# Kernel optimization log

Measured on AMD Instinct MI355X. Metric: run time of the kernel, lower is better.

The kernel has to match this reference:

```python
import jax, jax.numpy as jnp
import numpy as np
import math

HIDDEN = 1024
N_HEADS = 16
N_KV = 4
HEAD_DIM = HIDDEN // N_HEADS  # 64
B, S = 2, 2048
THETA = 100000.0


def _freqs_cos_sin(dim, end, theta):
    # yarn params: original_max_position_embeddings=2048 >= end, so no ramp scaling,
    # attention_factor=1.0 -> plain RoPE frequencies.
    inv = 1.0 / theta ** (np.arange(0, dim, 2)[: dim // 2] / dim)
    t = np.arange(end)
    f = np.outer(t, inv).astype(np.float32)  # (end, dim/2)
    cos = np.concatenate([np.cos(f), np.cos(f)], axis=-1)  # (end, dim)
    sin = np.concatenate([np.sin(f), np.sin(f)], axis=-1)
    return jnp.asarray(cos), jnp.asarray(sin)


def _rotate(x):
    # stack([-x[...,1::2], x[...,::2]], -1).reshape_as(x)
    return jnp.stack([-x[..., 1::2], x[..., ::2]], axis=-1).reshape(x.shape)


def setup_inputs() -> dict:
    key = jax.random.key(0)
    ks = jax.random.split(key, 9)
    s = 0.02
    return {
        "hidden_states": jax.random.normal(ks[0], (B, S, HIDDEN), jnp.float32),
        "attention_mask": jnp.ones((B, S), jnp.int32),
        "Wq": jax.random.normal(ks[1], (HIDDEN, HIDDEN), jnp.float32) * s,
        "bq": jnp.zeros((HIDDEN,), jnp.float32),
        "Wk": jax.random.normal(ks[2], (HIDDEN, N_KV * HEAD_DIM), jnp.float32) * s,
        "bk": jnp.zeros((N_KV * HEAD_DIM,), jnp.float32),
        "Wv": jax.random.normal(ks[3], (HIDDEN, N_KV * HEAD_DIM), jnp.float32) * s,
        "bv": jnp.zeros((N_KV * HEAD_DIM,), jnp.float32),
        "Wo": jax.random.normal(ks[4], (HIDDEN, HIDDEN), jnp.float32) * s,
        "bo": jnp.zeros((HIDDEN,), jnp.float32),
    }


def reference(hidden_states, attention_mask, Wq, bq, Wk, bk, Wv, bv, Wo, bo):
    b, s, _ = hidden_states.shape
    q = (hidden_states @ Wq + bq).reshape(b, s, N_HEADS, HEAD_DIM)
    k = (hidden_states @ Wk + bk).reshape(b, s, N_KV, HEAD_DIM)
    v = (hidden_states @ Wv + bv).reshape(b, s, N_KV, HEAD_DIM)

    cos, sin = _freqs_cos_sin(HEAD_DIM, s, THETA)
    cos = cos[:, None, :]  # (s,1,d) broadcasts over (b,s,h,d)
    sin = sin[:, None, :]
    q = q * cos + _rotate(q) * sin
    k = k * cos + _rotate(k) * sin

    # GQA: repeat_interleave kv heads -> jnp.repeat along head axis
    rep = N_HEADS // N_KV
    k = jnp.repeat(k, rep, axis=2)
    v = jnp.repeat(v, rep, axis=2)

    scores = jnp.einsum("bqhd,bkhd->bhqk", q, k) / math.sqrt(HEAD_DIM)
    neg = jnp.finfo(scores.dtype).min
    causal = jnp.triu(jnp.ones((s, s), bool), k=1)  # (q,kv)
    bias = jnp.where(causal, neg, 0.0).astype(scores.dtype)[None, None]
    key_mask = attention_mask.astype(bool)[:, None, None, :]  # (b,1,1,kv)
    bias = jnp.where(key_mask, bias, neg)
    probs = jax.nn.softmax(scores + bias, axis=-1)
    attn = jnp.einsum("bhqk,bkhd->bqhd", probs, v).reshape(b, s, HIDDEN)
    return attn @ Wo + bo
```

## Files before the change

kernel.cpp:

```cpp
#include <hip/hip_runtime.h>
#include <cstddef>
#include <cstdint>

#define B_   2
#define S_   2048
#define HID  1024
#define NH_  16
#define NKV_ 4
#define DH_  64
#define ROWS (B_ * S_)
#define NQKV 1536
#define QSCALE 0.18033688011112042f

typedef __bf16 bf16_t;
typedef _Float16 f16_t;
typedef bf16_t bf16x8 __attribute__((ext_vector_type(8)));
typedef bf16_t bf16x4 __attribute__((ext_vector_type(4)));
typedef f16_t  f16x8  __attribute__((ext_vector_type(8)));
typedef f16_t  f16x4  __attribute__((ext_vector_type(4)));
typedef float  f32x4  __attribute__((ext_vector_type(4)));

typedef __attribute__((address_space(1))) const uint32_t gu32_t;
typedef __attribute__((address_space(3))) uint32_t lu32_t;

__device__ __forceinline__ void gl_lds16(const void* g, void* l) {
  __builtin_amdgcn_global_load_lds((gu32_t*)g, (lu32_t*)l, 16, 0, 0);
}

__global__ void prep_all(const float* __restrict__ hs,
                         const float* __restrict__ Wq, const float* __restrict__ Wk,
                         const float* __restrict__ Wv, const float* __restrict__ Wo,
                         const float* __restrict__ bq, const float* __restrict__ bk,
                         const float* __restrict__ bv,
                         bf16_t* __restrict__ hsb,
                         bf16_t* __restrict__ Wt, bf16_t* __restrict__ Wot,
                         float* __restrict__ ball, float2* __restrict__ lut)
{
  const int bid = blockIdx.x;
  if (bid < 2048) {
    const int i = (bid * 256 + threadIdx.x) * 8;
    float4 a = *(const float4*)(hs + i);
    float4 b = *(const float4*)(hs + i + 4);
    bf16x8 o;
    o[0]=(bf16_t)a.x; o[1]=(bf16_t)a.y; o[2]=(bf16_t)a.z; o[3]=(bf16_t)a.w;
    o[4]=(bf16_t)b.x; o[5]=(bf16_t)b.y; o[6]=(bf16_t)b.z; o[7]=(bf16_t)b.w;
    *(bf16x8*)(hsb + i) = o;
    return;
  }
  if (bid >= 4614) {
    const int idx = (bid - 4614) * 256 + threadIdx.x;
    const int s = idx >> 5, j = idx & 31;
    const float L = 0.51905126482615037f;
    const float ang = (float)s * exp2f(-L * (float)j);
    lut[idx] = make_float2(cosf(ang), sinf(ang));
    return;
  }
  if (bid >= 4608) {
    int i = (bid - 4608) * 256 + threadIdx.x;
    if (i < NQKV) ball[i] = (i < 1024) ? bq[i] : ((i < 1280) ? bk[i-1024] : bv[i-1280]);
    return;
  }
  const int wb = bid - 2048;
  const float* src; bf16_t* dst; int N, n0, k0;
  if (wb < 1024)      { src = Wq; dst = Wt;            N = 1024; int t = wb;      n0=(t&31)*32; k0=(t>>5)*32; }
  else if (wb < 1280) { src = Wk; dst = Wt + 1024*HID; N = 256;  int t = wb-1024; n0=(t&7)*32;  k0=(t>>3)*32; }
  else if (wb < 1536) { src = Wv; dst = Wt + 1280*HID; N = 256;  int t = wb-1280; n0=(t&7)*32;  k0=(t>>3)*32; }
  else                { src = Wo; dst = Wot;           N = 1024; int t = wb-1536; n0=(t&31)*32; k0=(t>>5)*32; }
  __shared__ bf16_t T[32][33];
  const int tx = threadIdx.x & 31, ty = threadIdx.x >> 5;
#pragma unroll
  for (int i = 0; i < 4; ++i)
    T[ty + i*8][tx] = (bf16_t)src[(size_t)(k0 + ty + i*8) * N + n0 + tx];
  __syncthreads();
#pragma unroll
  for (int i = 0; i < 4; ++i)
    dst[(size_t)(n0 + ty + i*8) * HID + k0 + tx] = T[tx][ty + i*8];
}

__global__ __launch_bounds__(256, 3) void gemm64_b16o(
    const bf16_t* __restrict__ A, const bf16_t* __restrict__ Bt,
    const float* __restrict__ bias, bf16_t* __restrict__ C, int N)
{
  __shared__ bf16_t As[2][128 * 64];
  __shared__ bf16_t Bs[2][64 * 64];
  const int tid  = threadIdx.x;
  const int w    = tid >> 6;
  const int lane = tid & 63;
  const int m    = lane & 15;
  const int quad = lane >> 4;
  const int wm   = w >> 1, wn = w & 1;
  const size_t bm = (size_t)blockIdx.y * 128;
  const size_t bn = (size_t)blockIdx.x * 64;

  const int srow = w * 8 + (lane >> 3);
  const int scol = (lane & 7) * 8;
  const bf16_t* Ag = A  + (bm + srow) * HID + scol;
  const bf16_t* Bg = Bt + (bn + srow) * HID + scol;

  f32x4 acc[4][2];
#pragma unroll
  for (int i = 0; i < 4; ++i)
#pragma unroll
    for (int j = 0; j < 2; ++j) acc[i][j] = (f32x4){0.f, 0.f, 0.f, 0.f};

#pragma unroll
  for (int i = 0; i < 4; ++i)
    gl_lds16(Ag + (size_t)(i * 32) * HID, &As[0][(w * 8 + i * 32) * 64]);
#pragma unroll
  for (int i = 0; i < 2; ++i)
    gl_lds16(Bg + (size_t)(i * 32) * HID, &Bs[0][(w * 8 + i * 32) * 64]);

  int p = 0;
  for (int k0 = 0; k0 < HID; k0 += 64) {
    __syncthreads();
    if (k0 + 64 < HID) {
#pragma unroll
      for (int i = 0; i < 4; ++i)
        gl_lds16(Ag + (size_t)(i * 32) * HID + k0 + 64, &As[p^1][(w * 8 + i * 32) * 64]);
#pragma unroll
      for (int i = 0; i < 2; ++i)
        gl_lds16(Bg + (size_t)(i * 32) * HID + k0 + 64, &Bs[p^1][(w * 8 + i * 32) * 64]);
    }
#pragma unroll
    for (int ks = 0; ks < 2; ++ks) {
      bf16x8 af[4], bfr[2];
#pragma unroll
      for (int mt = 0; mt < 4; ++mt)
        af[mt] = *(const bf16x8*)&As[p][(wm * 64 + mt * 16 + m) * 64 + ks * 32 + quad * 8];
#pragma unroll
      for (int nt = 0; nt < 2; ++nt)
        bfr[nt] = *(const bf16x8*)&Bs[p][(wn * 32 + nt * 16 + m) * 64 + ks * 32 + quad * 8];
#pragma unroll
      for (int mt = 0; mt < 4; ++mt)
#pragma unroll
        for (int nt = 0; nt < 2; ++nt)
          acc[mt][nt] = __builtin_amdgcn_mfma_f32_16x16x32_bf16(bfr[nt], af[mt], acc[mt][nt], 0, 0, 0);
    }
    p ^= 1;
  }
#pragma unroll
  for (int mt = 0; mt < 4; ++mt) {
    const size_t row = bm + wm * 64 + mt * 16 + m;
#pragma unroll
    for (int nt = 0; nt < 2; ++nt) {
      const size_t col = bn + wn * 32 + nt * 16 + quad * 4;
      float4 bb = *(const float4*)&bias[col];
      bf16x4 o;
      o[0] = (bf16_t)(acc[mt][nt][0] + bb.x);
      o[1] = (bf16_t)(acc[mt][nt][1] + bb.y);
      o[2] = (bf16_t)(acc[mt][nt][2] + bb.z);
      o[3] = (bf16_t)(acc[mt][nt][3] + bb.w);
      *(bf16x4*)&C[row * N + col] = o;
    }
  }
}

__global__ __launch_bounds__(256, 3) void gemm64_f32o(
    const bf16_t* __restrict__ A, const bf16_t* __restrict__ Bt,
    const float* __restrict__ bias, float* __restrict__ C, int N)
{
  __shared__ bf16_t As[2][128 * 64];
  __shared__ bf16_t Bs[2][64 * 64];
  const int tid  = threadIdx.x;
  const int w    = tid >> 6;
  const int lane = tid & 63;
  const int m    = lane & 15;
  const int quad = lane >> 4;
  const int wm   = w >> 1, wn = w & 1;
  const size_t bm = (size_t)blockIdx.y * 128;
  const size_t bn = (size_t)blockIdx.x * 64;

  const int srow = w * 8 + (lane >> 3);
  const int scol = (lane & 7) * 8;
  const bf16_t* Ag = A  + (bm + srow) * HID + scol;
  const bf16_t* Bg = Bt + (bn + srow) * HID + scol;

  f32x4 acc[4][2];
#pragma unroll
  for (int i = 0; i < 4; ++i)
#pragma unroll
    for (int j = 0; j < 2; ++j) acc[i][j] = (f32x4){0.f, 0.f, 0.f, 0.f};

#pragma unroll
  for (int i = 0; i < 4; ++i)
    gl_lds16(Ag + (size_t)(i * 32) * HID, &As[0][(w * 8 + i * 32) * 64]);
#pragma unroll
  for (int i = 0; i < 2; ++i)
    gl_lds16(Bg + (size_t)(i * 32) * HID, &Bs[0][(w * 8 + i * 32) * 64]);

  int p = 0;
  for (int k0 = 0; k0 < HID; k0 += 64) {
    __syncthreads();
    if (k0 + 64 < HID) {
#pragma unroll
      for (int i = 0; i < 4; ++i)
        gl_lds16(Ag + (size_t)(i * 32) * HID + k0 + 64, &As[p^1][(w * 8 + i * 32) * 64]);
#pragma unroll
      for (int i = 0; i < 2; ++i)
        gl_lds16(Bg + (size_t)(i * 32) * HID + k0 + 64, &Bs[p^1][(w * 8 + i * 32) * 64]);
    }
#pragma unroll
    for (int ks = 0; ks < 2; ++ks) {
      bf16x8 af[4], bfr[2];
#pragma unroll
      for (int mt = 0; mt < 4; ++mt)
        af[mt] = *(const bf16x8*)&As[p][(wm * 64 + mt * 16 + m) * 64 + ks * 32 + quad * 8];
#pragma unroll
      for (int nt = 0; nt < 2; ++nt)
        bfr[nt] = *(const bf16x8*)&Bs[p][(wn * 32 + nt * 16 + m) * 64 + ks * 32 + quad * 8];
#pragma unroll
      for (int mt = 0; mt < 4; ++mt)
#pragma unroll
        for (int nt = 0; nt < 2; ++nt)
          acc[mt][nt] = __builtin_amdgcn_mfma_f32_16x16x32_bf16(bfr[nt], af[mt], acc[mt][nt], 0, 0, 0);
    }
    p ^= 1;
  }
#pragma unroll
  for (int mt = 0; mt < 4; ++mt) {
    const size_t row = bm + wm * 64 + mt * 16 + m;
#pragma unroll
    for (int nt = 0; nt < 2; ++nt) {
      const size_t col = bn + wn * 32 + nt * 16 + quad * 4;
      float4 bb = *(const float4*)&bias[col];
      float4 o;
      o.x = acc[mt][nt][0] + bb.x; o.y = acc[mt][nt][1] + bb.y;
      o.z = acc[mt][nt][2] + bb.z; o.w = acc[mt][nt][3] + bb.w;
      *(float4*)&C[row * N + col] = o;
    }
  }
}

__global__ void prep_kv(const bf16_t* __restrict__ QKVb, const float2* __restrict__ lut,
                        bf16_t* __restrict__ Kimg, f16_t* __restrict__ Vimg)
{
  __shared__ bf16_t Lk[64][72];
  __shared__ bf16_t Lv[64][72];
  const int bid = blockIdx.x, t = threadIdx.x;
  const int kt = bid & 31, kvh = (bid >> 5) & 3, b = bid >> 7;
  const size_t img = ((size_t)(b * NKV_ + kvh) * 32 + kt) * 4096;

  {
    const int r0 = t >> 3, c8 = (t & 7) * 8;
#pragma unroll
    for (int i = 0; i < 2; ++i) {
      const int r = r0 + i * 32;
      const bf16_t* src = QKVb + (size_t)(b * S_ + kt * 64 + r) * NQKV + 1024 + kvh * DH_ + c8;
      *(bf16x8*)&Lk[r][c8] = *(const bf16x8*)src;
      *(bf16x8*)&Lv[r][c8] = *(const bf16x8*)(src + 256);
    }
  }
  __syncthreads();
  {
    const int key = t & 63, cg = t >> 6;
    const int srow = kt * 64 + key;
    bf16x8 a = *(const bf16x8*)&Lk[key][cg * 16];
    bf16x8 c = *(const bf16x8*)&Lk[key][cg * 16 + 8];
    const float2* lp = lut + srow * 32 + ((cg & 1) * 16);
    float v[16];
#pragma unroll
    for (int i = 0; i < 8; ++i) { v[i] = (float)a[i]; v[i + 8] = (float)c[i]; }
    bf16x8 o0, o1;
#pragma unroll
    for (int j = 0; j < 8; ++j) {
      const float2 ce = lp[2 * j], co = lp[2 * j + 1];
      const float y0 = v[2*j] * ce.x - v[2*j+1] * ce.y;
      const float y1 = v[2*j+1] * co.x + v[2*j] * co.y;
      if (j < 4) { o0[2*j] = (bf16_t)y0; o0[2*j+1] = (bf16_t)y1; }
      else       { o1[2*(j-4)] = (bf16_t)y0; o1[2*(j-4)+1] = (bf16_t)y1; }
    }
    const int s0 = (2 * cg) ^ (key & 7);
    *(bf16x8*)&Kimg[img + key * 64 + s0 * 8]       = o0;
    *(bf16x8*)&Kimg[img + key * 64 + (s0 ^ 1) * 8] = o1;
  }
  {
    const int d = t & 63, cg = t >> 6;
#pragma unroll
    for (int g4 = 0; g4 < 4; ++g4) {
      const int g = cg * 4 + g4;
      f16x4 o;
#pragma unroll
      for (int j = 0; j < 4; ++j)
        o[j] = (f16_t)(float)Lv[g * 4 + j][d];
      const int slot = g ^ (d & 15);
      *(f16x4*)&Vimg[img + d * 64 + slot * 4] = o;
    }
  }
}

__global__ __launch_bounds__(256, 4) void attn_v7(
    const bf16_t* __restrict__ QKVb, const float2* __restrict__ lut,
    const bf16_t* __restrict__ Kt2, const f16_t* __restrict__ Vt2,
    const int* __restrict__ amask, bf16_t* __restrict__ Ab)
{
  __shared__ __align__(16) bf16_t Ks[2][64 * 64];
  __shared__ __align__(16) f16_t  Vs[2][64 * 64];

  const int tid  = threadIdx.x;
  const int w    = tid >> 6;
  const int lane = tid & 63;
  const int m    = lane & 15;
  const int quad = lane >> 4;
  const int kvh  = blockIdx.y;
  const int b    = blockIdx.z;
  const int h    = kvh * 4 + w;
  const int qt   = 127 - blockIdx.x;
  const int q0w  = qt * 16;
  const int nkt  = (q0w >> 6) + 1;

  bf16x8 aq[2];
  {
    const int spos = q0w + m;
    const bf16_t* qsrc = QKVb + (size_t)(b * S_ + spos) * NQKV + h * DH_;
    float2 l8[8];
#pragma unroll
    for (int j = 0; j < 8; ++j) l8[j] = lut[spos * 32 + quad * 8 + j];
#pragma unroll
    for (int kc = 0; kc < 2; ++kc) {
      bf16x8 x = *(const bf16x8*)(qsrc + kc * 32 + quad * 8);
      bf16x8 y;
#pragma unroll
      for (int i = 0; i < 4; ++i) {
        const float x0 = (float)x[2*i], x1 = (float)x[2*i+1];
        y[2*i]   = (bf16_t)((x0 * l8[2*i].x   - x1 * l8[2*i].y)   * QSCALE);
        y[2*i+1] = (bf16_t)((x1 * l8[2*i+1].x + x0 * l8[2*i+1].y) * QSCALE);
      }
      aq[kc] = y;
    }
  }

  f32x4 oacc[4];
#pragma unroll
  for (int d = 0; d < 4; ++d) oacc[d] = (f32x4){0.f,0.f,0.f,0.f};
  float lpart = 0.f;

  const size_t imgbase = ((size_t)(b * NKV_ + kvh) * 32) * 4096;
  const bf16_t* Kg = Kt2 + imgbase;
  const f16_t*  Vg = Vt2 + imgbase;
  const int x0s = quad ^ (m & 7);
  const int x1s = (4 + quad) ^ (m & 7);
  const int* amp = amask + b * S_;

  gl_lds16(Kg + (2*w)   * 512 + lane * 8, &Ks[0][(2*w)   * 512]);
  gl_lds16(Kg + (2*w+1) * 512 + lane * 8, &Ks[0][(2*w+1) * 512]);
  gl_lds16(Vg + (2*w)   * 512 + lane * 8, &Vs[0][(2*w)   * 512]);
  gl_lds16(Vg + (2*w+1) * 512 + lane * 8, &Vs[0][(2*w+1) * 512]);
  int mcur = amp[lane];

  int p = 0;
  for (int kt = 0; kt < nkt; ++kt) {
    const int kbase = kt * 64;
    __syncthreads();
    const bool more = (kt + 1 < nkt);
    if (more) {
      const size_t off = (size_t)(kt + 1) * 4096;
      gl_lds16(Kg + off + (2*w)   * 512 + lane * 8, &Ks[p^1][(2*w)   * 512]);
      gl_lds16(Kg + off + (2*w+1) * 512 + lane * 8, &Ks[p^1][(2*w+1) * 512]);
      gl_lds16(Vg + off + (2*w)   * 512 + lane * 8, &Vs[p^1][(2*w)   * 512]);
      gl_lds16(Vg + off + (2*w+1) * 512 + lane * 8, &Vs[p^1][(2*w+1) * 512]);
    }
    int mnext = more ? amp[(kt + 1) * 64 + lane] : 0;
    const uint64_t mb = __ballot(mcur != 0);

    f32x4 sc[4];
#pragma unroll
    for (int cb = 0; cb < 4; ++cb) sc[cb] = (f32x4){0.f,0.f,0.f,0.f};
#pragma unroll
    for (int cb = 0; cb < 4; ++cb) {
      const bf16x8 bk0 = *(const bf16x8*)&Ks[p][(cb*16 + m) * 64 + x0s * 8];
      const bf16x8 bk1 = *(const bf16x8*)&Ks[p][(cb*16 + m) * 64 + x1s * 8];
      sc[cb] = __builtin_amdgcn_mfma_f32_16x16x32_bf16(bk0, aq[0], sc[cb], 0, 0, 0);
      sc[cb] = __builtin_amdgcn_mfma_f32_16x16x32_bf16(bk1, aq[1], sc[cb], 0, 0, 0);
    }

    f16x4 bp[4];
    {
      const bool needm = (kbase + 63 > q0w) || (mb != ~0ull);
      if (needm) {
        const int qv = q0w + m;
#pragma unroll
        for (int cb = 0; cb < 4; ++cb)
#pragma unroll
          for (int r = 0; r < 4; ++r) {
            const int idx = cb*16 + quad*4 + r;
            const bool ok = (kbase + idx <= qv) && ((mb >> idx) & 1);
            sc[cb][r] = ok ? sc[cb][r] : -1e38f;
          }
      }
      float sum = 0.f;
#pragma unroll
      for (int cb = 0; cb < 4; ++cb) {
        f16x4 pp;
#pragma unroll
        for (int r = 0; r < 4; ++r) {
          const float pv = exp2f(sc[cb][r]);
          sum += pv;
          pp[r] = (f16_t)pv;
        }
        bp[cb] = pp;
      }
      lpart += sum;
    }

#pragma unroll
    for (int cb = 0; cb < 4; ++cb) {
      f16x4 av[4];
#pragma unroll
      for (int dblk = 0; dblk < 4; ++dblk) {
        const int slot = (cb * 4 + quad) ^ m;
        av[dblk] = *(const f16x4*)&Vs[p][(dblk*16 + m) * 64 + slot * 4];
      }
#pragma unroll
      for (int dblk = 0; dblk < 4; ++dblk)
        oacc[dblk] = __builtin_amdgcn_mfma_f32_16x16x16f16(av[dblk], bp[cb], oacc[dblk], 0, 0, 0);
    }
    mcur = mnext;
    p ^= 1;
  }

  {
    float l = lpart;
    l += __shfl_xor(l, 16);
    l += __shfl_xor(l, 32);
    const float inv = 1.0f / l;
    const size_t row = (size_t)(b * S_ + q0w + m);
#pragma unroll
    for (int dblk = 0; dblk < 4; ++dblk) {
      bf16x4 o;
      o[0] = (bf16_t)(oacc[dblk][0] * inv);
      o[1] = (bf16_t)(oacc[dblk][1] * inv);
      o[2] = (bf16_t)(oacc[dblk][2] * inv);
      o[3] = (bf16_t)(oacc[dblk][3] * inv);
      *(bf16x4*)&Ab[row * HID + h * DH_ + dblk * 16 + quad * 4] = o;
    }
  }
}

extern "C" void kernel_launch(void* const* d_in, const int* in_sizes, int n_in,
                              void* d_out, int out_size, void* d_ws, size_t ws_size,
                              hipStream_t stream)
{
  const float* hs    = (const float*)d_in[0];
  const int*   amask = (const int*)  d_in[1];
  const float* Wq    = (const float*)d_in[2];
  const float* bq    = (const float*)d_in[3];
  const float* Wk    = (const float*)d_in[4];
  const float* bk    = (const float*)d_in[5];
  const float* Wv    = (const float*)d_in[6];
  const float* bv    = (const float*)d_in[7];
  const float* Wo    = (const float*)d_in[8];
  const float* bo    = (const float*)d_in[9];
  float* out = (float*)d_out;

  bf16_t* QKVb = (bf16_t*)d_ws;
  bf16_t* hsb  = QKVb + (size_t)ROWS * NQKV;
  bf16_t* Wt   = hsb + (size_t)ROWS * HID;
  bf16_t* Wot  = Wt + (size_t)NQKV * HID;
  float*  ball = (float*)(Wot + (size_t)HID * HID);
  bf16_t* Kimg = (bf16_t*)(ball + NQKV);
  f16_t*  Vimg = (f16_t*)(Kimg + (size_t)B_*NKV_*32*4096);
  float2* lut  = (float2*)(Vimg + (size_t)B_*NKV_*32*4096);
  bf16_t* Ab   = hsb;

  prep_all<<<4870, 256, 0, stream>>>(hs, Wq, Wk, Wv, Wo, bq, bk, bv,
                                     hsb, Wt, Wot, ball, lut);

  gemm64_b16o<<<dim3(NQKV/64, ROWS/128), 256, 0, stream>>>(hsb, Wt, ball, QKVb, NQKV);

  prep_kv<<<256, 256, 0, stream>>>(QKVb, lut, Kimg, Vimg);

  attn_v7<<<dim3(128, NKV_, B_), 256, 0, stream>>>(QKVb, lut, Kimg, Vimg, amask, Ab);

  gemm64_f32o<<<dim3(HID/64, ROWS/128), 256, 0, stream>>>(Ab, Wot, bo, out, HID);
}
```

Baseline: 198.7 us.

## Pair complementary causal query tiles per block and split KV across wave groups

The attention kernel now gives each block two query tiles, one short causal row x and its complement 127-x. This balances the number of KV tiles per block and halves the grid to 64x4x2 with 512 threads. The combined KV tile sequence of both query tiles is interleaved across two 4-wave groups, each with its own double-buffered LDS K/V staging. Both groups keep partial accumulators for both tiles, so the partial outputs and row sums are exchanged through LDS and merged before normalization and the final store. This is meant to remove the causal load imbalance and long tail, at the cost of doubled LDS use, more registers for two accumulator sets, and an extra reduction step through LDS.

New measurement: 187.9 us. -5.4%, faster.

```diff
diff --git a/kernel.cpp b/kernel.cpp
--- a/kernel.cpp
+++ b/kernel.cpp
@@ -288,51 +288,107 @@
   }
 }
 
-__global__ __launch_bounds__(256, 4) void attn_v7(
+#define PROC_TILE(AQ, OACC, LP, Q0W)                                          \
+  do {                                                                        \
+    f32x4 sc[4];                                                              \
+    _Pragma("unroll") for (int cb = 0; cb < 4; ++cb)                          \
+      sc[cb] = (f32x4){0.f, 0.f, 0.f, 0.f};                                   \
+    _Pragma("unroll") for (int cb = 0; cb < 4; ++cb) {                        \
+      const bf16x8 bk0 = *(const bf16x8*)&Ks[g][p][(cb*16 + m) * 64 + x0s * 8]; \
+      const bf16x8 bk1 = *(const bf16x8*)&Ks[g][p][(cb*16 + m) * 64 + x1s * 8]; \
+      sc[cb] = __builtin_amdgcn_mfma_f32_16x16x32_bf16(bk0, AQ[0], sc[cb], 0, 0, 0); \
+      sc[cb] = __builtin_amdgcn_mfma_f32_16x16x32_bf16(bk1, AQ[1], sc[cb], 0, 0, 0); \
+    }                                                                         \
+    f16x4 bp[4];                                                              \
+    {                                                                         \
+      const bool needm = (kbase + 63 > (Q0W)) || (mb != ~0ull);               \
+      if (needm) {                                                            \
+        const int qv = (Q0W) + m;                                             \
+        _Pragma("unroll") for (int cb = 0; cb < 4; ++cb)                      \
+          _Pragma("unroll") for (int r = 0; r < 4; ++r) {                     \
+            const int idx = cb*16 + quad*4 + r;                               \
+            const bool ok = (kbase + idx <= qv) && ((mb >> idx) & 1);         \
+            sc[cb][r] = ok ? sc[cb][r] : -1e38f;                              \
+          }                                                                   \
+      }                                                                       \
+      float sum = 0.f;                                                        \
+      _Pragma("unroll") for (int cb = 0; cb < 4; ++cb) {                      \
+        f16x4 pp;                                                             \
+        _Pragma("unroll") for (int r = 0; r < 4; ++r) {                       \
+          const float pv = exp2f(sc[cb][r]);                                  \
+          sum += pv;                                                          \
+          pp[r] = (f16_t)pv;                                                  \
+        }                                                                     \
+        bp[cb] = pp;                                                          \
+      }                                                                       \
+      LP += sum;                                                              \
+    }                                                                         \
+    _Pragma("unroll") for (int cb = 0; cb < 4; ++cb) {                        \
+      f16x4 av[4];                                                            \
+      _Pragma("unroll") for (int dblk = 0; dblk < 4; ++dblk) {                \
+        const int slot = (cb * 4 + quad) ^ m;                                 \
+        av[dblk] = *(const f16x4*)&Vs[g][p][(dblk*16 + m) * 64 + slot * 4];   \
+      }                                                                       \
+      _Pragma("unroll") for (int dblk = 0; dblk < 4; ++dblk)                  \
+        OACC[dblk] = __builtin_amdgcn_mfma_f32_16x16x16f16(av[dblk], bp[cb], OACC[dblk], 0, 0, 0); \
+    }                                                                         \
+  } while (0)
+
+__global__ __launch_bounds__(512, 4) void attn_v8(
     const bf16_t* __restrict__ QKVb, const float2* __restrict__ lut,
     const bf16_t* __restrict__ Kt2, const f16_t* __restrict__ Vt2,
     const int* __restrict__ amask, bf16_t* __restrict__ Ab)
 {
-  __shared__ __align__(16) bf16_t Ks[2][64 * 64];
-  __shared__ __align__(16) f16_t  Vs[2][64 * 64];
+  __shared__ __align__(16) bf16_t Ks[2][2][64 * 64];
+  __shared__ __align__(16) f16_t  Vs[2][2][64 * 64];
 
   const int tid  = threadIdx.x;
   const int w    = tid >> 6;
+  const int g    = w >> 2;
+  const int wl   = w & 3;
   const int lane = tid & 63;
   const int m    = lane & 15;
   const int quad = lane >> 4;
   const int kvh  = blockIdx.y;
   const int b    = blockIdx.z;
-  const int h    = kvh * 4 + w;
-  const int qt   = 127 - blockIdx.x;
-  const int q0w  = qt * 16;
-  const int nkt  = (q0w >> 6) + 1;
-
-  bf16x8 aq[2];
-  {
-    const int spos = q0w + m;
+  const int h    = kvh * 4 + wl;
+  const int x    = blockIdx.x;
+  const int q0wA = x * 16;
+  const int q0wB = (127 - x) * 16;
+  const int nA   = (x >> 2) + 1;
+  const int nB   = ((127 - x) >> 2) + 1;
+  const int T    = nA + nB;
+
+  bf16x8 aqA[2], aqB[2];
+#pragma unroll
+  for (int tt = 0; tt < 2; ++tt) {
+    const int q0w_t = tt ? q0wB : q0wA;
+    const int spos = q0w_t + m;
     const bf16_t* qsrc = QKVb + (size_t)(b * S_ + spos) * NQKV + h * DH_;
     float2 l8[8];
 #pragma unroll
     for (int j = 0; j < 8; ++j) l8[j] = lut[spos * 32 + quad * 8 + j];
 #pragma unroll
     for (int kc = 0; kc < 2; ++kc) {
-      bf16x8 x = *(const bf16x8*)(qsrc + kc * 32 + quad * 8);
+      bf16x8 xv = *(const bf16x8*)(qsrc + kc * 32 + quad * 8);
       bf16x8 y;
 #pragma unroll
       for (int i = 0; i < 4; ++i) {
-        const float x0 = (float)x[2*i], x1 = (float)x[2*i+1];
+        const float x0 = (float)xv[2*i], x1 = (float)xv[2*i+1];
         y[2*i]   = (bf16_t)((x0 * l8[2*i].x   - x1 * l8[2*i].y)   * QSCALE);
         y[2*i+1] = (bf16_t)((x1 * l8[2*i+1].x + x0 * l8[2*i+1].y) * QSCALE);
       }
-      aq[kc] = y;
-    }
-  }
-
-  f32x4 oacc[4];
-#pragma unroll
-  for (int d = 0; d < 4; ++d) oacc[d] = (f32x4){0.f,0.f,0.f,0.f};
-  float lpart = 0.f;
+      if (tt) aqB[kc] = y; else aqA[kc] = y;
+    }
+  }
+
+  f32x4 oaccA[4], oaccB[4];
+#pragma unroll
+  for (int d = 0; d < 4; ++d) {
+    oaccA[d] = (f32x4){0.f,0.f,0.f,0.f};
+    oaccB[d] = (f32x4){0.f,0.f,0.f,0.f};
+  }
+  float lpA = 0.f, lpB = 0.f;
 
   const size_t imgbase = ((size_t)(b * NKV_ + kvh) * 32) * 4096;
   const bf16_t* Kg = Kt2 + imgbase;
@@ -341,96 +397,96 @@
   const int x1s = (4 + quad) ^ (m & 7);
   const int* amp = amask + b * S_;
 
-  gl_lds16(Kg + (2*w)   * 512 + lane * 8, &Ks[0][(2*w)   * 512]);
-  gl_lds16(Kg + (2*w+1) * 512 + lane * 8, &Ks[0][(2*w+1) * 512]);
-  gl_lds16(Vg + (2*w)   * 512 + lane * 8, &Vs[0][(2*w)   * 512]);
-  gl_lds16(Vg + (2*w+1) * 512 + lane * 8, &Vs[0][(2*w+1) * 512]);
-  int mcur = amp[lane];
+  int mcur;
+  {
+    const int e0  = g;
+    const int kt0 = (e0 >= nA) ? e0 - nA : e0;
+    const size_t off = (size_t)kt0 * 4096;
+    gl_lds16(Kg + off + (2*wl)   * 512 + lane * 8, &Ks[g][0][(2*wl)   * 512]);
+    gl_lds16(Kg + off + (2*wl+1) * 512 + lane * 8, &Ks[g][0][(2*wl+1) * 512]);
+    gl_lds16(Vg + off + (2*wl)   * 512 + lane * 8, &Vs[g][0][(2*wl)   * 512]);
+    gl_lds16(Vg + off + (2*wl+1) * 512 + lane * 8, &Vs[g][0][(2*wl+1) * 512]);
+    mcur = amp[kt0 * 64 + lane];
+  }
 
   int p = 0;
-  for (int kt = 0; kt < nkt; ++kt) {
-    const int kbase = kt * 64;
+  const int niter = (T + 1) >> 1;
+  for (int t = 0; t < niter; ++t) {
+    const int e = 2 * t + g;
     __syncthreads();
-    const bool more = (kt + 1 < nkt);
+    const int e2 = e + 2;
+    const bool more = (e2 < T);
+    int kt2 = 0;
     if (more) {
-      const size_t off = (size_t)(kt + 1) * 4096;
-      gl_lds16(Kg + off + (2*w)   * 512 + lane * 8, &Ks[p^1][(2*w)   * 512]);
-      gl_lds16(Kg + off + (2*w+1) * 512 + lane * 8, &Ks[p^1][(2*w+1) * 512]);
-      gl_lds16(Vg + off + (2*w)   * 512 + lane * 8, &Vs[p^1][(2*w)   * 512]);
-      gl_lds16(Vg + off + (2*w+1) * 512 + lane * 8, &Vs[p^1][(2*w+1) * 512]);
-    }
-    int mnext = more ? amp[(kt + 1) * 64 + lane] : 0;
-    const uint64_t mb = __ballot(mcur != 0);
-
-    f32x4 sc[4];
-#pragma unroll
-    for (int cb = 0; cb < 4; ++cb) sc[cb] = (f32x4){0.f,0.f,0.f,0.f};
-#pragma unroll
-    for (int cb = 0; cb < 4; ++cb) {
-      const bf16x8 bk0 = *(const bf16x8*)&Ks[p][(cb*16 + m) * 64 + x0s * 8];
-      const bf16x8 bk1 = *(const bf16x8*)&Ks[p][(cb*16 + m) * 64 + x1s * 8];
-      sc[cb] = __builtin_amdgcn_mfma_f32_16x16x32_bf16(bk0, aq[0], sc[cb], 0, 0, 0);
-      sc[cb] = __builtin_amdgcn_mfma_f32_16x16x32_bf16(bk1, aq[1], sc[cb], 0, 0, 0);
-    }
-
-    f16x4 bp[4];
-    {
-      const bool needm = (kbase + 63 > q0w) || (mb != ~0ull);
-      if (needm) {
-        const int qv = q0w + m;
-#pragma unroll
-        for (int cb = 0; cb < 4; ++cb)
-#pragma unroll
-          for (int r = 0; r < 4; ++r) {
-            const int idx = cb*16 + quad*4 + r;
-            const bool ok = (kbase + idx <= qv) && ((mb >> idx) & 1);
-            sc[cb][r] = ok ? sc[cb][r] : -1e38f;
-          }
-      }
-      float sum = 0.f;
-#pragma unroll
-      for (int cb = 0; cb < 4; ++cb) {
-        f16x4 pp;
-#pragma unroll
-        for (int r = 0; r < 4; ++r) {
-          const float pv = exp2f(sc[cb][r]);
-          sum += pv;
-          pp[r] = (f16_t)pv;
-        }
-        bp[cb] = pp;
-      }
-      lpart += sum;
-    }
-
-#pragma unroll
-    for (int cb = 0; cb < 4; ++cb) {
-      f16x4 av[4];
-#pragma unroll
-      for (int dblk = 0; dblk < 4; ++dblk) {
-        const int slot = (cb * 4 + quad) ^ m;
-        av[dblk] = *(const f16x4*)&Vs[p][(dblk*16 + m) * 64 + slot * 4];
-      }
-#pragma unroll
-      for (int dblk = 0; dblk < 4; ++dblk)
-        oacc[dblk] = __builtin_amdgcn_mfma_f32_16x16x16f16(av[dblk], bp[cb], oacc[dblk], 0, 0, 0);
+      kt2 = (e2 >= nA) ? e2 - nA : e2;
+      const size_t off = (size_t)kt2 * 4096;
+      gl_lds16(Kg + off + (2*wl)   * 512 + lane * 8, &Ks[g][p^1][(2*wl)   * 512]);
+      gl_lds16(Kg + off + (2*wl+1) * 512 + lane * 8, &Ks[g][p^1][(2*wl+1) * 512]);
+      gl_lds16(Vg + off + (2*wl)   * 512 + lane * 8, &Vs[g][p^1][(2*wl)   * 512]);
+      gl_lds16(Vg + off + (2*wl+1) * 512 + lane * 8, &Vs[g][p^1][(2*wl+1) * 512]);
+    }
+    const int mnext = more ? amp[kt2 * 64 + lane] : 0;
+    if (e < T) {
+      const uint64_t mb = __ballot(mcur != 0);
+      const bool isB = (e >= nA);
+      const int kt = isB ? e - nA : e;
+      const int kbase = kt * 64;
+      if (isB) PROC_TILE(aqB, oaccB, lpB, q0wB);
+      else     PROC_TILE(aqA, oaccA, lpA, q0wA);
     }
     mcur = mnext;
     p ^= 1;
   }
 
-  {
-    float l = lpart;
-    l += __shfl_xor(l, 16);
-    l += __shfl_xor(l, 32);
+  float lAred = lpA;
+  lAred += __shfl_xor(lAred, 16); lAred += __shfl_xor(lAred, 32);
+  float lBred = lpB;
+  lBred += __shfl_xor(lBred, 16); lBred += __shfl_xor(lBred, 32);
+
+  __syncthreads();
+  float* scrA = (float*)&Ks[0][0][0];
+  float* scrB = (float*)&Vs[0][0][0];
+  const int sbase = wl * 1104 + m * 68 + quad * 4;
+
+  if (g == 0) {
+#pragma unroll
+    for (int dblk = 0; dblk < 4; ++dblk)
+      *(f32x4*)&scrA[sbase + dblk * 16] = oaccA[dblk];
+    if (quad == 0) scrA[wl * 1104 + 16 * 68 + m] = lAred;
+  } else {
+#pragma unroll
+    for (int dblk = 0; dblk < 4; ++dblk)
+      *(f32x4*)&scrB[sbase + dblk * 16] = oaccB[dblk];
+    if (quad == 0) scrB[wl * 1104 + 16 * 68 + m] = lBred;
+  }
+  __syncthreads();
+
+  if (g == 0) {
+    const float l = lBred + scrB[wl * 1104 + 16 * 68 + m];
     const float inv = 1.0f / l;
-    const size_t row = (size_t)(b * S_ + q0w + m);
+    const size_t row = (size_t)(b * S_ + q0wB + m);
 #pragma unroll
     for (int dblk = 0; dblk < 4; ++dblk) {
+      const f32x4 part = *(const f32x4*)&scrB[sbase + dblk * 16];
       bf16x4 o;
-      o[0] = (bf16_t)(oacc[dblk][0] * inv);
-      o[1] = (bf16_t)(oacc[dblk][1] * inv);
-      o[2] = (bf16_t)(oacc[dblk][2] * inv);
-      o[3] = (bf16_t)(oacc[dblk][3] * inv);
+      o[0] = (bf16_t)((oaccB[dblk][0] + part[0]) * inv);
+      o[1] = (bf16_t)((oaccB[dblk][1] + part[1]) * inv);
+      o[2] = (bf16_t)((oaccB[dblk][2] + part[2]) * inv);
+      o[3] = (bf16_t)((oaccB[dblk][3] + part[3]) * inv);
+      *(bf16x4*)&Ab[row * HID + h * DH_ + dblk * 16 + quad * 4] = o;
+    }
+  } else {
+    const float l = lAred + scrA[wl * 1104 + 16 * 68 + m];
+    const float inv = 1.0f / l;
+    const size_t row = (size_t)(b * S_ + q0wA + m);
+#pragma unroll
+    for (int dblk = 0; dblk < 4; ++dblk) {
+      const f32x4 part = *(const f32x4*)&scrA[sbase + dblk * 16];
+      bf16x4 o;
+      o[0] = (bf16_t)((oaccA[dblk][0] + part[0]) * inv);
+      o[1] = (bf16_t)((oaccA[dblk][1] + part[1]) * inv);
+      o[2] = (bf16_t)((oaccA[dblk][2] + part[2]) * inv);
+      o[3] = (bf16_t)((oaccA[dblk][3] + part[3]) * inv);
       *(bf16x4*)&Ab[row * HID + h * DH_ + dblk * 16 + quad * 4] = o;
     }
   }
@@ -469,7 +525,7 @@
 
   prep_kv<<<256, 256, 0, stream>>>(QKVb, lut, Kimg, Vimg);
 
-  attn_v7<<<dim3(128, NKV_, B_), 256, 0, stream>>>(QKVb, lut, Kimg, Vimg, amask, Ab);
+  attn_v8<<<dim3(64, NKV_, B_), 512, 0, stream>>>(QKVb, lut, Kimg, Vimg, amask, Ab);
 
   gemm64_f32o<<<dim3(HID/64, ROWS/128), 256, 0, stream>>>(Ab, Wot, bo, out, HID);
 }
```
